# Performance work log

Measured on AMD Instinct MI355X. Metric: run time of the kernel, lower is better.

Reference implementation:

```python
import jax, jax.numpy as jnp
import numpy as np

N_FFT = 4096
HOP = 1024
WIN = 4096
DIAG_EPS = 1e-7
EPS = 1e-8

# asteroid-style periodic sqrt-hann analysis/synthesis window
_n = np.arange(WIN)
WINDOW = jnp.asarray(np.sqrt(0.5 - 0.5 * np.cos(2.0 * np.pi * _n / WIN)), dtype=jnp.float32)


def _frame_idx(n_samp):
    T = (n_samp - WIN) // HOP + 1
    return np.arange(T)[:, None] * HOP + np.arange(WIN)[None, :]


def stft(x):
    """x: (..., N) -> (real, imag) each (..., F, T) with F = N_FFT//2+1."""
    idx = _frame_idx(x.shape[-1])
    frames = x[..., idx] * WINDOW
    spec = jnp.fft.rfft(frames, axis=-1)     # (..., T, F) complex64
    spec = jnp.moveaxis(spec, -2, -1)        # (..., F, T)
    return spec.real, spec.imag


def istft(re, im, out_len):
    """(..., F, T) -> (..., out_len) via windowed overlap-add."""
    spec = jnp.moveaxis(re + 1j * im, -1, -2)            # (..., T, F)
    frames = jnp.fft.irfft(spec, n=WIN, axis=-1) * WINDOW
    T = frames.shape[-2]
    full = (T - 1) * HOP + WIN
    idx = _frame_idx(full).reshape(-1)
    flat = frames.reshape(frames.shape[:-2] + (-1,))
    out = jnp.zeros(frames.shape[:-2] + (full,), frames.dtype).at[..., idx].add(flat)
    wsq = jnp.zeros((full,), jnp.float32).at[idx].add(jnp.tile(WINDOW ** 2, T))
    out = out / jnp.maximum(wsq, 1e-8)
    return out[..., :out_len]


def psd_causal(re, im):
    """Causal, frame-normalized PSD. re/im: (B, C, F, T) -> complex (B, T, F, C, C)."""
    pr = jnp.einsum('saft,sbft->sabft', re, re) + jnp.einsum('saft,sbft->sabft', im, im)
    pi = jnp.einsum('saft,sbft->sbaft', re, im) - jnp.einsum('saft,sbft->sabft', re, im)
    cnt = jnp.arange(1, re.shape[-1] + 1, dtype=re.dtype)
    pr = jnp.cumsum(pr, -1) / cnt
    pi = jnp.cumsum(pi, -1) / cnt
    psd = pr + 1j * pi                       # (B, a, b, F, T)
    return jnp.transpose(psd, (0, 4, 3, 1, 2))  # (B, T, F, C, C)


def mvdr_vector(psd_s, psd_n):
    """Souden MVDR: ws = inv(Npsd) @ Spsd / (tr(.) + eps). (..., C, C) complex."""
    C = psd_n.shape[-1]
    tr_n = jnp.trace(psd_n, axis1=-2, axis2=-1).real
    epsilon = jax.lax.stop_gradient(tr_n * DIAG_EPS + EPS)
    psd_n = psd_n + epsilon[..., None, None] * jnp.eye(C, dtype=psd_n.dtype)
    num = jnp.linalg.inv(psd_n) @ psd_s
    return num / (jnp.trace(num, axis1=-2, axis2=-1)[..., None, None] + EPS)


def _forward(x, s):
    B, S, C, N = s.shape
    xs = jnp.broadcast_to(x[:, None], (B, S, C, N)).reshape(B * S, C, N)
    ss = s.reshape(B * S, C, N)
    Xr, Xi = stft(xs)
    Sr, Si = stft(ss)
    Nr, Ni = Xr - Sr, Xi - Si
    Sscm = psd_causal(Sr, Si)   # (BS, T, F, C, C)
    Nscm = psd_causal(Nr, Ni)
    ws = mvdr_vector(Sscm, Nscm)  # (BS, T, F, C, C)
    # conj(filter), rearranged to (BS, a, b, F, T)
    fr = jnp.transpose(ws.real, (0, 3, 4, 2, 1))
    fi = -jnp.transpose(ws.imag, (0, 3, 4, 2, 1))
    enh_r = jnp.einsum('sabft,saft->sbft', fr, Xr) - jnp.einsum('sabft,saft->sbft', fi, Xi)
    enh_i = jnp.einsum('sabft,saft->sbft', fr, Xi) + jnp.einsum('sabft,saft->sbft', fi, Xr)
    est = istft(enh_r, enh_i, N)            # (BS, C, N)
    return est.reshape(B, S, C, N)


def setup_inputs() -> dict:
    key = jax.random.key(0)
    kx, ks = jax.random.split(key)
    x = jax.random.normal(kx, (2, 4, 32768), dtype=jnp.float32)
    s = jax.random.normal(ks, (2, 2, 4, 32768), dtype=jnp.float32)
    return {"x": x, "s": s, "do_permute": 0}


def reference(x, s, do_permute):
    # do_permute=False path (PIT permutation is a data-dependent preprocessing step)
    return _forward(x, s)
```

## Files before the change

kernel.cpp:

```cpp
#include <hip/hip_runtime.h>

static constexpr int NFFT = 4096;
static constexpr int HOP  = 1024;
static constexpr int NF   = 2049;
static constexpr int NT   = 29;
static constexpr int NS   = 32768;
static constexpr int NB   = 2;
static constexpr int NSrc = 2;
static constexpr int NC   = 4;
static constexpr int NBS  = NB * NSrc;
static constexpr int FCHUNKS = (NF + 7) / 8;

#define PI_F     3.14159265358979323846f
#define TWO_PI_F 6.28318530717958647692f

#define IDX(a) ((a) + ((a) >> 4))
static constexpr int LDSN = 2048 + 128;

__device__ inline float2 cmul(float2 a, float2 b) {
    return make_float2(a.x * b.x - a.y * b.y, a.x * b.y + a.y * b.x);
}
__device__ inline float2 cmulc(float2 a, float2 b) {
    return make_float2(a.x * b.x + a.y * b.y, a.y * b.x - a.x * b.y);
}

template <int CTRL, int RMASK>
__device__ __forceinline__ float dpp0(float x) {
    return __int_as_float(__builtin_amdgcn_update_dpp(
        0, __float_as_int(x), CTRL, RMASK, 0xF, true));
}

template <int DIR>
__device__ inline void fft4v(float2 v[4]) {
    float2 t0 = make_float2(v[0].x + v[2].x, v[0].y + v[2].y);
    float2 t1 = make_float2(v[0].x - v[2].x, v[0].y - v[2].y);
    float2 t2 = make_float2(v[1].x + v[3].x, v[1].y + v[3].y);
    float2 t3 = make_float2(v[1].x - v[3].x, v[1].y - v[3].y);
    v[0] = make_float2(t0.x + t2.x, t0.y + t2.y);
    v[2] = make_float2(t0.x - t2.x, t0.y - t2.y);
    if (DIR < 0) {
        v[1] = make_float2(t1.x + t3.y, t1.y - t3.x);
        v[3] = make_float2(t1.x - t3.y, t1.y + t3.x);
    } else {
        v[1] = make_float2(t1.x - t3.y, t1.y + t3.x);
        v[3] = make_float2(t1.x + t3.y, t1.y - t3.x);
    }
}

template <int DIR>
__device__ inline void fft8v(float2 v[8]) {
    float2 e[4] = { v[0], v[2], v[4], v[6] };
    float2 o[4] = { v[1], v[3], v[5], v[7] };
    fft4v<DIR>(e);
    fft4v<DIR>(o);
    const float c = 0.70710678118654752f;
    float2 o0 = o[0], o1, o2, o3;
    if (DIR < 0) {
        o1 = make_float2(c * (o[1].x + o[1].y), c * (o[1].y - o[1].x));
        o2 = make_float2(o[2].y, -o[2].x);
        o3 = make_float2(c * (o[3].y - o[3].x), -c * (o[3].x + o[3].y));
    } else {
        o1 = make_float2(c * (o[1].x - o[1].y), c * (o[1].y + o[1].x));
        o2 = make_float2(-o[2].y, o[2].x);
        o3 = make_float2(-c * (o[3].x + o[3].y), c * (o[3].x - o[3].y));
    }
    v[0] = make_float2(e[0].x + o0.x, e[0].y + o0.y);
    v[4] = make_float2(e[0].x - o0.x, e[0].y - o0.y);
    v[1] = make_float2(e[1].x + o1.x, e[1].y + o1.y);
    v[5] = make_float2(e[1].x - o1.x, e[1].y - o1.y);
    v[2] = make_float2(e[2].x + o2.x, e[2].y + o2.y);
    v[6] = make_float2(e[2].x - o2.x, e[2].y - o2.y);
    v[3] = make_float2(e[3].x + o3.x, e[3].y + o3.y);
    v[7] = make_float2(e[3].x - o3.x, e[3].y - o3.y);
}

template <int DIR, int NSs>
__device__ inline void stage8(const float* __restrict__ reS, const float* __restrict__ imS,
                              float* __restrict__ reD, float* __restrict__ imD, int tid) {
    int j = tid;
    float2 v[8];
    #pragma unroll
    for (int r = 0; r < 8; ++r) {
        int a = IDX(j + (r << 8));
        v[r] = make_float2(reS[a], imS[a]);
    }
    if (NSs > 1) {
        float ang = (float)DIR * (TWO_PI_F / (8.0f * (float)NSs)) * (float)(j & (NSs - 1));
        float2 w1; __sincosf(ang, &w1.y, &w1.x);
        float2 w2 = cmul(w1, w1);
        float2 w3 = cmul(w2, w1);
        float2 w4 = cmul(w2, w2);
        float2 w5 = cmul(w3, w2);
        float2 w6 = cmul(w3, w3);
        float2 w7 = cmul(w4, w3);
        v[1] = cmul(v[1], w1);
        v[2] = cmul(v[2], w2);
        v[3] = cmul(v[3], w3);
        v[4] = cmul(v[4], w4);
        v[5] = cmul(v[5], w5);
        v[6] = cmul(v[6], w6);
        v[7] = cmul(v[7], w7);
    }
    fft8v<DIR>(v);
    int idxD = ((j & ~(NSs - 1)) << 3) + (j & (NSs - 1));
    #pragma unroll
    for (int r = 0; r < 8; ++r) {
        int a = IDX(idxD + r * NSs);
        reD[a] = v[r].x;
        imD[a] = v[r].y;
    }
}

template <int DIR>
__device__ inline void stage4_512(const float* __restrict__ reS, const float* __restrict__ imS,
                                  float* __restrict__ reD, float* __restrict__ imD, int tid) {
    #pragma unroll
    for (int h = 0; h < 2; ++h) {
        int j = tid + (h << 8);
        float2 v[4];
        #pragma unroll
        for (int r = 0; r < 4; ++r) {
            int a = IDX(j + (r << 9));
            v[r] = make_float2(reS[a], imS[a]);
        }
        float ang = (float)DIR * (TWO_PI_F / 2048.0f) * (float)j;
        float2 w1; __sincosf(ang, &w1.y, &w1.x);
        float2 w2 = cmul(w1, w1);
        float2 w3 = cmul(w2, w1);
        v[1] = cmul(v[1], w1);
        v[2] = cmul(v[2], w2);
        v[3] = cmul(v[3], w3);
        fft4v<DIR>(v);
        #pragma unroll
        for (int r = 0; r < 4; ++r) {
            int a = IDX(j + (r << 9));
            reD[a] = v[r].x;
            imD[a] = v[r].y;
        }
    }
}

template <int DIR>
__device__ inline void fft2048(float* reA, float* imA, float* reB, float* imB, int tid) {
    stage8<DIR, 1>(reA, imA, reB, imB, tid);  __syncthreads();
    stage8<DIR, 8>(reB, imB, reA, imA, tid);  __syncthreads();
    stage8<DIR, 64>(reA, imA, reB, imB, tid); __syncthreads();
    stage4_512<DIR>(reB, imB, reA, imA, tid); __syncthreads();
}

__global__ __launch_bounds__(256) void stft_kernel(
    const float* __restrict__ x, const float* __restrict__ s,
    float2* __restrict__ Xs, float2* __restrict__ Ss) {
    __shared__ float reA[LDSN], imA[LDSN], reB[LDSN], imB[LDSN];
    int tid = threadIdx.x;
    int fid = blockIdx.x;
    const float* src;
    float2* dst;
    if (fid < NB * NC * NT) {
        int b = fid / (NC * NT);
        int r = fid % (NC * NT);
        int c = r / NT;
        int t = r % NT;
        src = x + (size_t)((b * NC + c) * NS + t * HOP);
        dst = Xs + (size_t)((b * NC + c) * NT + t) * NF;
    } else {
        int g  = fid - NB * NC * NT;
        int bs = g / (NC * NT);
        int r  = g % (NC * NT);
        int c  = r / NT;
        int t  = r % NT;
        src = s + (size_t)((bs * NC + c) * NS + t * HOP);
        dst = Ss + (size_t)((bs * NC + c) * NT + t) * NF;
    }
    const float2* s2 = (const float2*)src;
    for (int n = tid; n < 2048; n += 256) {
        float2 v = s2[n];
        float we = __sinf((float)n * (PI_F / 2048.0f));
        float wo = __sinf((float)(2 * n + 1) * (PI_F / 4096.0f));
        int a = IDX(n);
        reA[a] = v.x * we;
        imA[a] = v.y * wo;
    }
    __syncthreads();
    fft2048<-1>(reA, imA, reB, imB, tid);
    for (int k = tid; k <= 1024; k += 256) {
        int a1 = IDX(k);
        int a2 = IDX((2048 - k) & 2047);
        float2 Za = make_float2(reA[a1], imA[a1]);
        float2 Zb = make_float2(reA[a2], imA[a2]);
        if (k == 0) {
            dst[0]    = make_float2(Za.x + Za.y, 0.f);
            dst[2048] = make_float2(Za.x - Za.y, 0.f);
        } else {
            float2 Ze = make_float2(0.5f * (Za.x + Zb.x),  0.5f * (Za.y - Zb.y));
            float2 Zo = make_float2(0.5f * (Za.y + Zb.y), -0.5f * (Za.x - Zb.x));
            float ang = -(PI_F / 2048.0f) * (float)k;
            float2 W; __sincosf(ang, &W.y, &W.x);
            float2 WZo = cmul(W, Zo);
            dst[k] = make_float2(Ze.x + WZo.x, Ze.y + WZo.y);
            if (k < 1024)
                dst[2048 - k] = make_float2(Ze.x - WZo.x, -(Ze.y - WZo.y));
        }
    }
}

__global__ __launch_bounds__(256) void mvdr2_kernel(
    const float2* __restrict__ Xs, const float2* __restrict__ Ss,
    float2* __restrict__ Es) {
    int tid   = threadIdx.x;
    int blk   = blockIdx.x;
    int bs    = blk / FCHUNKS;
    int f0    = (blk % FCHUNKS) * 8;
    int b     = bs >> 1;
    int lane  = tid & 63;
    int wave  = tid >> 6;
    int t     = lane & 31;
    int fpair = lane >> 5;
    int fi    = wave * 2 + fpair;
    int f     = f0 + fi;
    bool valid = (t < NT) && (f < NF);

    float2 Sv[4], Xv[4], Nv[4];
    #pragma unroll
    for (int c = 0; c < 4; ++c) {
        if (valid) {
            Sv[c] = Ss[(size_t)((bs * NC + c) * NT + t) * NF + f];
            Xv[c] = Xs[(size_t)((b  * NC + c) * NT + t) * NF + f];
        } else {
            Sv[c] = make_float2(0.f, 0.f);
            Xv[c] = make_float2(0.f, 0.f);
        }
        Nv[c] = make_float2(Xv[c].x - Sv[c].x, Xv[c].y - Sv[c].y);
    }

    float v[32];
    #pragma unroll
    for (int c = 0; c < 4; ++c) {
        v[c]      = Sv[c].x * Sv[c].x + Sv[c].y * Sv[c].y;
        v[16 + c] = Nv[c].x * Nv[c].x + Nv[c].y * Nv[c].y;
    }
    constexpr int PI6[6] = {0, 0, 0, 1, 1, 2};
    constexpr int PJ6[6] = {1, 2, 3, 2, 3, 3};
    #pragma unroll
    for (int p = 0; p < 6; ++p) {
        float2 d = cmulc(Sv[PI6[p]], Sv[PJ6[p]]);
        v[4 + 2 * p] = d.x; v[5 + 2 * p] = d.y;
        d = cmulc(Nv[PI6[p]], Nv[PJ6[p]]);
        v[20 + 2 * p] = d.x; v[21 + 2 * p] = d.y;
    }

    #pragma unroll
    for (int k = 0; k < 32; ++k) v[k] += dpp0<0x111, 0xF>(v[k]);
    #pragma unroll
    for (int k = 0; k < 32; ++k) v[k] += dpp0<0x112, 0xF>(v[k]);
    #pragma unroll
    for (int k = 0; k < 32; ++k) v[k] += dpp0<0x114, 0xF>(v[k]);
    #pragma unroll
    for (int k = 0; k < 32; ++k) v[k] += dpp0<0x118, 0xF>(v[k]);
    #pragma unroll
    for (int k = 0; k < 32; ++k) v[k] += dpp0<0x142, 0xA>(v[k]);

    float pd0 = v[0], pd1 = v[1], pd2 = v[2], pd3 = v[3];
    float2 po0 = make_float2(v[4],  v[5]);
    float2 po1 = make_float2(v[6],  v[7]);
    float2 po2 = make_float2(v[8],  v[9]);
    float2 po3 = make_float2(v[10], v[11]);
    float2 po4 = make_float2(v[12], v[13]);
    float2 po5 = make_float2(v[14], v[15]);
    float eps = (v[16] + v[17] + v[18] + v[19]) * 1e-7f + (float)(t + 1) * 1e-8f;
    float nd0 = v[16] + eps, nd1 = v[17] + eps, nd2 = v[18] + eps, nd3 = v[19] + eps;
    float2 no0 = make_float2(v[20], v[21]);
    float2 no1 = make_float2(v[22], v[23]);
    float2 no2 = make_float2(v[24], v[25]);
    float2 no3 = make_float2(v[26], v[27]);
    float2 no4 = make_float2(v[28], v[29]);
    float2 no5 = make_float2(v[30], v[31]);

    float D0 = nd0;
    float r0 = __builtin_amdgcn_rcpf(D0);
    float2 L10 = make_float2(no0.x * r0, -no0.y * r0);
    float2 L20 = make_float2(no1.x * r0, -no1.y * r0);
    float2 L30 = make_float2(no2.x * r0, -no2.y * r0);
    float D1 = nd1 - (L10.x * L10.x + L10.y * L10.y) * D0;
    float r1 = __builtin_amdgcn_rcpf(D1);
    float2 c10 = make_float2(D0 * L10.x, -D0 * L10.y);
    float2 tA = cmul(L20, c10);
    float2 L21 = make_float2((no3.x - tA.x) * r1, (-no3.y - tA.y) * r1);
    float2 tB = cmul(L30, c10);
    float2 L31 = make_float2((no4.x - tB.x) * r1, (-no4.y - tB.y) * r1);
    float D2 = nd2 - (L20.x * L20.x + L20.y * L20.y) * D0
                   - (L21.x * L21.x + L21.y * L21.y) * D1;
    float r2 = __builtin_amdgcn_rcpf(D2);
    float2 c20 = make_float2(D0 * L20.x, -D0 * L20.y);
    float2 c21 = make_float2(D1 * L21.x, -D1 * L21.y);
    float2 tC = cmul(L30, c20);
    float2 tD = cmul(L31, c21);
    float2 L32 = make_float2((no5.x - tC.x - tD.x) * r2, (-no5.y - tC.y - tD.y) * r2);
    float D3 = nd3 - (L30.x * L30.x + L30.y * L30.y) * D0
                   - (L31.x * L31.x + L31.y * L31.y) * D1
                   - (L32.x * L32.x + L32.y * L32.y) * D2;
    float r3 = __builtin_amdgcn_rcpf(D3);

    float2 u0 = Xv[0];
    float2 m0 = cmul(L10, u0);
    float2 u1 = make_float2(Xv[1].x - m0.x, Xv[1].y - m0.y);
    float2 m1 = cmul(L20, u0), m2 = cmul(L21, u1);
    float2 u2 = make_float2(Xv[2].x - m1.x - m2.x, Xv[2].y - m1.y - m2.y);
    float2 m3 = cmul(L30, u0), m4 = cmul(L31, u1), m5 = cmul(L32, u2);
    float2 u3 = make_float2(Xv[3].x - m3.x - m4.x - m5.x,
                            Xv[3].y - m3.y - m4.y - m5.y);
    float2 w0 = make_float2(u0.x * r0, u0.y * r0);
    float2 w1 = make_float2(u1.x * r1, u1.y * r1);
    float2 w2 = make_float2(u2.x * r2, u2.y * r2);
    float2 w3 = make_float2(u3.x * r3, u3.y * r3);
    float2 z3 = w3;
    float2 n0_ = cmulc(z3, L32);
    float2 z2 = make_float2(w2.x - n0_.x, w2.y - n0_.y);
    float2 n1_ = cmulc(z2, L21), n2_ = cmulc(z3, L31);
    float2 z1 = make_float2(w1.x - n1_.x - n2_.x, w1.y - n1_.y - n2_.y);
    float2 n3_ = cmulc(z1, L10), n4_ = cmulc(z2, L20), n5_ = cmulc(z3, L30);
    float2 z0 = make_float2(w0.x - n3_.x - n4_.x - n5_.x,
                            w0.y - n3_.y - n4_.y - n5_.y);

    float2 K10 = make_float2(-L10.x, -L10.y);
    float2 kk  = cmul(L21, L10);
    float2 K20 = make_float2(kk.x - L20.x, kk.y - L20.y);
    float2 K21 = make_float2(-L21.x, -L21.y);
    kk = cmul(L32, L21);
    float2 K31 = make_float2(kk.x - L31.x, kk.y - L31.y);
    float2 K32 = make_float2(-L32.x, -L32.y);
    float2 ka = cmul(K31, L10), kb = cmul(L32, L20);
    float2 K30 = make_float2(-L30.x - ka.x + kb.x, -L30.y - ka.y + kb.y);

    float q0 = pd0;
    float2 qm = cmul(K10, po0);
    float q1 = pd1 + (K10.x * K10.x + K10.y * K10.y) * pd0 + 2.0f * qm.x;
    qm = cmul(K20, po0);
    float s_a = qm.x * K21.x + qm.y * K21.y;
    qm = cmul(K20, po1);
    float s_b = qm.x;
    qm = cmul(K21, po3);
    float s_c = qm.x;
    float q2 = pd2 + (K20.x * K20.x + K20.y * K20.y) * pd0
                   + (K21.x * K21.x + K21.y * K21.y) * pd1
                   + 2.0f * (s_a + s_b + s_c);
    qm = cmul(K30, po0);
    float s1 = qm.x * K31.x + qm.y * K31.y;
    qm = cmul(K30, po1);
    float s2 = qm.x * K32.x + qm.y * K32.y;
    qm = cmul(K30, po2);
    float s3 = qm.x;
    qm = cmul(K31, po3);
    float s4 = qm.x * K32.x + qm.y * K32.y;
    qm = cmul(K31, po4);
    float s5 = qm.x;
    qm = cmul(K32, po5);
    float s6 = qm.x;
    float q3 = pd3 + (K30.x * K30.x + K30.y * K30.y) * pd0
                   + (K31.x * K31.x + K31.y * K31.y) * pd1
                   + (K32.x * K32.x + K32.y * K32.y) * pd2
                   + 2.0f * (s1 + s2 + s3 + s4 + s5 + s6);
    float tr = q0 * r0 + q1 * r1 + q2 * r2 + q3 * r3;
    float g  = __builtin_amdgcn_rcpf(tr + 1e-8f);

    float2 a0 = cmul(po0, z1), a1 = cmul(po1, z2), a2 = cmul(po2, z3);
    float2 e0 = make_float2(pd0 * z0.x + a0.x + a1.x + a2.x,
                            pd0 * z0.y + a0.y + a1.y + a2.y);
    a0 = cmulc(z0, po0); a1 = cmul(po3, z2); a2 = cmul(po4, z3);
    float2 e1 = make_float2(a0.x + pd1 * z1.x + a1.x + a2.x,
                            a0.y + pd1 * z1.y + a1.y + a2.y);
    a0 = cmulc(z0, po1); a1 = cmulc(z1, po3); a2 = cmul(po5, z3);
    float2 e2 = make_float2(a0.x + a1.x + pd2 * z2.x + a2.x,
                            a0.y + a1.y + pd2 * z2.y + a2.y);
    a0 = cmulc(z0, po2); a1 = cmulc(z1, po4); a2 = cmulc(z2, po5);
    float2 e3 = make_float2(a0.x + a1.x + a2.x + pd3 * z3.x,
                            a0.y + a1.y + a2.y + pd3 * z3.y);
    if (valid) {
        Es[(size_t)((bs * NC + 0) * NT + t) * NF + f] = make_float2(e0.x * g, e0.y * g);
        Es[(size_t)((bs * NC + 1) * NT + t) * NF + f] = make_float2(e1.x * g, e1.y * g);
        Es[(size_t)((bs * NC + 2) * NT + t) * NF + f] = make_float2(e2.x * g, e2.y * g);
        Es[(size_t)((bs * NC + 3) * NT + t) * NF + f] = make_float2(e3.x * g, e3.y * g);
    }
}

__global__ __launch_bounds__(256) void istft_kernel(
    const float2* __restrict__ Es, float* __restrict__ Fr) {
    __shared__ float reA[LDSN], imA[LDSN], reB[LDSN], imB[LDSN];
    int tid = threadIdx.x;
    int fid = blockIdx.x;
    int bs = fid / (NC * NT);
    int r  = fid % (NC * NT);
    int c  = r / NT;
    int t  = r % NT;
    const float2* src = Es + (size_t)((bs * NC + c) * NT + t) * NF;
    for (int k = tid; k <= 1024; k += 256) {
        float2 A = src[k];
        float2 B = src[2048 - k];
        float2 Ze = make_float2(0.5f * (A.x + B.x), 0.5f * (A.y - B.y));
        float2 D  = make_float2(0.5f * (A.x - B.x), 0.5f * (A.y + B.y));
        float ang = (PI_F / 2048.0f) * (float)k;
        float2 W; __sincosf(ang, &W.y, &W.x);
        float2 Zo = cmul(W, D);
        int a1 = IDX(k);
        reA[a1] = Ze.x - Zo.y;
        imA[a1] = Ze.y + Zo.x;
        if (k > 0 && k < 1024) {
            int a2 = IDX(2048 - k);
            reA[a2] = Ze.x + Zo.y;
            imA[a2] = -Ze.y + Zo.x;
        }
    }
    __syncthreads();
    fft2048<1>(reA, imA, reB, imB, tid);
    float2* d2 = (float2*)(Fr + (size_t)((bs * NC + c) * NT + t) * NFFT);
    for (int n = tid; n < 2048; n += 256) {
        int a = IDX(n);
        float we = __sinf((float)n * (PI_F / 2048.0f)) * (1.0f / 2048.0f);
        float wo = __sinf((float)(2 * n + 1) * (PI_F / 4096.0f)) * (1.0f / 2048.0f);
        d2[n] = make_float2(reA[a] * we, imA[a] * wo);
    }
}

__global__ __launch_bounds__(256) void ola_kernel(
    const float* __restrict__ Fr, float* __restrict__ out) {
    int idx = blockIdx.x * 256 + threadIdx.x;
    const int total = NBS * NC * NS;
    if (idx >= total) return;
    int p  = idx & (NS - 1);
    int ch = idx >> 15;
    int t1 = p >> 10;
    if (t1 > NT - 1) t1 = NT - 1;
    int t0 = (p >= NFFT) ? ((p - (NFFT - 1) + (HOP - 1)) >> 10) : 0;
    float acc = 0.f;
    for (int t = t0; t <= t1; ++t)
        acc += Fr[((size_t)(ch * NT + t) << 12) + (p - (t << 10))];
    float wacc;
    if (t1 - t0 == 3) {
        wacc = 2.0f;
    } else {
        wacc = 0.f;
        for (int t = t0; t <= t1; ++t) {
            float w = __sinf((float)(p - (t << 10)) * (PI_F / 4096.0f));
            wacc += w * w;
        }
    }
    out[idx] = acc / fmaxf(wacc, 1e-8f);
}

extern "C" void kernel_launch(void* const* d_in, const int* in_sizes, int n_in,
                              void* d_out, int out_size, void* d_ws, size_t ws_size,
                              hipStream_t stream) {
    const float* x = (const float*)d_in[0];
    const float* s = (const float*)d_in[1];
    float* out = (float*)d_out;

    const size_t XS_N = (size_t)NB  * NC * NT * NF;
    const size_t SS_N = (size_t)NBS * NC * NT * NF;
    float2* Xs = (float2*)d_ws;
    float2* Ss = Xs + XS_N;
    float2* Es = Ss + SS_N;
    float*  Fr = (float*)(Es + SS_N);

    stft_kernel<<<NB * NC * NT + NBS * NC * NT, 256, 0, stream>>>(x, s, Xs, Ss);

    mvdr2_kernel<<<NBS * FCHUNKS, 256, 0, stream>>>(Xs, Ss, Es);

    istft_kernel<<<NBS * NC * NT, 256, 0, stream>>>(Es, Fr);

    int ola_total = NBS * NC * NS;
    ola_kernel<<<(ola_total + 255) / 256, 256, 0, stream>>>(Fr, out);
}
```

Measured before the change: 37.33 us.

## Pad spectra to even bin stride and process two bins per thread in MVDR

Spectra buffers now use a padded row stride of 2050 bins, so each MVDR thread can load and store two adjacent frequency bins with 16-byte vector accesses. The MVDR kernel is restructured to handle 16 bins per block, with the solve factored into a helper that runs twice per thread. This halves the block count and widens memory transactions, at the cost of doubled register pressure (64 reduction values) and a launch bound that may limit occupancy. It risks spilling and has fewer blocks to hide latency.

Result: slower. 38.11 us (+2.1%).

```diff
diff --git a/kernel.cpp b/kernel.cpp
--- a/kernel.cpp
+++ b/kernel.cpp
@@ -3,13 +3,14 @@
 static constexpr int NFFT = 4096;
 static constexpr int HOP  = 1024;
 static constexpr int NF   = 2049;
+static constexpr int NF2  = 2050;
 static constexpr int NT   = 29;
 static constexpr int NS   = 32768;
 static constexpr int NB   = 2;
 static constexpr int NSrc = 2;
 static constexpr int NC   = 4;
 static constexpr int NBS  = NB * NSrc;
-static constexpr int FCHUNKS = (NF + 7) / 8;
+static constexpr int FCH16 = 129;
 
 #define PI_F     3.14159265358979323846f
 #define TWO_PI_F 6.28318530717958647692f
@@ -162,7 +163,7 @@
         int c = r / NT;
         int t = r % NT;
         src = x + (size_t)((b * NC + c) * NS + t * HOP);
-        dst = Xs + (size_t)((b * NC + c) * NT + t) * NF;
+        dst = Xs + (size_t)((b * NC + c) * NT + t) * NF2;
     } else {
         int g  = fid - NB * NC * NT;
         int bs = g / (NC * NT);
@@ -170,7 +171,7 @@
         int c  = r / NT;
         int t  = r % NT;
         src = s + (size_t)((bs * NC + c) * NS + t * HOP);
-        dst = Ss + (size_t)((bs * NC + c) * NT + t) * NF;
+        dst = Ss + (size_t)((bs * NC + c) * NT + t) * NF2;
     }
     const float2* s2 = (const float2*)src;
     for (int n = tid; n < 2048; n += 256) {
@@ -204,62 +205,9 @@
     }
 }
 
-__global__ __launch_bounds__(256) void mvdr2_kernel(
-    const float2* __restrict__ Xs, const float2* __restrict__ Ss,
-    float2* __restrict__ Es) {
-    int tid   = threadIdx.x;
-    int blk   = blockIdx.x;
-    int bs    = blk / FCHUNKS;
-    int f0    = (blk % FCHUNKS) * 8;
-    int b     = bs >> 1;
-    int lane  = tid & 63;
-    int wave  = tid >> 6;
-    int t     = lane & 31;
-    int fpair = lane >> 5;
-    int fi    = wave * 2 + fpair;
-    int f     = f0 + fi;
-    bool valid = (t < NT) && (f < NF);
-
-    float2 Sv[4], Xv[4], Nv[4];
-    #pragma unroll
-    for (int c = 0; c < 4; ++c) {
-        if (valid) {
-            Sv[c] = Ss[(size_t)((bs * NC + c) * NT + t) * NF + f];
-            Xv[c] = Xs[(size_t)((b  * NC + c) * NT + t) * NF + f];
-        } else {
-            Sv[c] = make_float2(0.f, 0.f);
-            Xv[c] = make_float2(0.f, 0.f);
-        }
-        Nv[c] = make_float2(Xv[c].x - Sv[c].x, Xv[c].y - Sv[c].y);
-    }
-
-    float v[32];
-    #pragma unroll
-    for (int c = 0; c < 4; ++c) {
-        v[c]      = Sv[c].x * Sv[c].x + Sv[c].y * Sv[c].y;
-        v[16 + c] = Nv[c].x * Nv[c].x + Nv[c].y * Nv[c].y;
-    }
-    constexpr int PI6[6] = {0, 0, 0, 1, 1, 2};
-    constexpr int PJ6[6] = {1, 2, 3, 2, 3, 3};
-    #pragma unroll
-    for (int p = 0; p < 6; ++p) {
-        float2 d = cmulc(Sv[PI6[p]], Sv[PJ6[p]]);
-        v[4 + 2 * p] = d.x; v[5 + 2 * p] = d.y;
-        d = cmulc(Nv[PI6[p]], Nv[PJ6[p]]);
-        v[20 + 2 * p] = d.x; v[21 + 2 * p] = d.y;
-    }
-
-    #pragma unroll
-    for (int k = 0; k < 32; ++k) v[k] += dpp0<0x111, 0xF>(v[k]);
-    #pragma unroll
-    for (int k = 0; k < 32; ++k) v[k] += dpp0<0x112, 0xF>(v[k]);
-    #pragma unroll
-    for (int k = 0; k < 32; ++k) v[k] += dpp0<0x114, 0xF>(v[k]);
-    #pragma unroll
-    for (int k = 0; k < 32; ++k) v[k] += dpp0<0x118, 0xF>(v[k]);
-    #pragma unroll
-    for (int k = 0; k < 32; ++k) v[k] += dpp0<0x142, 0xA>(v[k]);
-
+__device__ __forceinline__ void mvdr_solve(const float* __restrict__ v,
+                                           const float2* __restrict__ Xv,
+                                           int t, float2* __restrict__ e) {
     float pd0 = v[0], pd1 = v[1], pd2 = v[2], pd3 = v[3];
     float2 po0 = make_float2(v[4],  v[5]);
     float2 po1 = make_float2(v[6],  v[7]);
@@ -364,22 +312,106 @@
     float g  = __builtin_amdgcn_rcpf(tr + 1e-8f);
 
     float2 a0 = cmul(po0, z1), a1 = cmul(po1, z2), a2 = cmul(po2, z3);
-    float2 e0 = make_float2(pd0 * z0.x + a0.x + a1.x + a2.x,
-                            pd0 * z0.y + a0.y + a1.y + a2.y);
+    e[0] = make_float2((pd0 * z0.x + a0.x + a1.x + a2.x) * g,
+                       (pd0 * z0.y + a0.y + a1.y + a2.y) * g);
     a0 = cmulc(z0, po0); a1 = cmul(po3, z2); a2 = cmul(po4, z3);
-    float2 e1 = make_float2(a0.x + pd1 * z1.x + a1.x + a2.x,
-                            a0.y + pd1 * z1.y + a1.y + a2.y);
+    e[1] = make_float2((a0.x + pd1 * z1.x + a1.x + a2.x) * g,
+                       (a0.y + pd1 * z1.y + a1.y + a2.y) * g);
     a0 = cmulc(z0, po1); a1 = cmulc(z1, po3); a2 = cmul(po5, z3);
-    float2 e2 = make_float2(a0.x + a1.x + pd2 * z2.x + a2.x,
-                            a0.y + a1.y + pd2 * z2.y + a2.y);
+    e[2] = make_float2((a0.x + a1.x + pd2 * z2.x + a2.x) * g,
+                       (a0.y + a1.y + pd2 * z2.y + a2.y) * g);
     a0 = cmulc(z0, po2); a1 = cmulc(z1, po4); a2 = cmulc(z2, po5);
-    float2 e3 = make_float2(a0.x + a1.x + a2.x + pd3 * z3.x,
-                            a0.y + a1.y + a2.y + pd3 * z3.y);
-    if (valid) {
-        Es[(size_t)((bs * NC + 0) * NT + t) * NF + f] = make_float2(e0.x * g, e0.y * g);
-        Es[(size_t)((bs * NC + 1) * NT + t) * NF + f] = make_float2(e1.x * g, e1.y * g);
-        Es[(size_t)((bs * NC + 2) * NT + t) * NF + f] = make_float2(e2.x * g, e2.y * g);
-        Es[(size_t)((bs * NC + 3) * NT + t) * NF + f] = make_float2(e3.x * g, e3.y * g);
+    e[3] = make_float2((a0.x + a1.x + a2.x + pd3 * z3.x) * g,
+                       (a0.y + a1.y + a2.y + pd3 * z3.y) * g);
+}
+
+__global__ __launch_bounds__(256, 1) void mvdr2_kernel(
+    const float2* __restrict__ Xs, const float2* __restrict__ Ss,
+    float2* __restrict__ Es) {
+    int tid   = threadIdx.x;
+    int blk   = blockIdx.x;
+    int bs    = blk / FCH16;
+    int f0    = (blk % FCH16) * 16;
+    int b     = bs >> 1;
+    int lane  = tid & 63;
+    int wave  = tid >> 6;
+    int t     = lane & 31;
+    int fpair = lane >> 5;
+    int fA    = f0 + (wave * 2 + fpair) * 2;
+    bool loadok = (t < NT) && (fA <= 2048);
+
+    float2 SvA[4], SvB[4], XvA[4], XvB[4];
+    #pragma unroll
+    for (int c = 0; c < 4; ++c) {
+        if (loadok) {
+            float4 qs = *(const float4*)&Ss[(size_t)((bs * NC + c) * NT + t) * NF2 + fA];
+            float4 qx = *(const float4*)&Xs[(size_t)((b  * NC + c) * NT + t) * NF2 + fA];
+            SvA[c] = make_float2(qs.x, qs.y);
+            SvB[c] = make_float2(qs.z, qs.w);
+            XvA[c] = make_float2(qx.x, qx.y);
+            XvB[c] = make_float2(qx.z, qx.w);
+        } else {
+            SvA[c] = make_float2(0.f, 0.f);
+            SvB[c] = make_float2(0.f, 0.f);
+            XvA[c] = make_float2(0.f, 0.f);
+            XvB[c] = make_float2(0.f, 0.f);
+        }
+    }
+    float2 NvA[4], NvB[4];
+    #pragma unroll
+    for (int c = 0; c < 4; ++c) {
+        NvA[c] = make_float2(XvA[c].x - SvA[c].x, XvA[c].y - SvA[c].y);
+        NvB[c] = make_float2(XvB[c].x - SvB[c].x, XvB[c].y - SvB[c].y);
+    }
+
+    float v[64];
+    #pragma unroll
+    for (int c = 0; c < 4; ++c) {
+        v[c]      = SvA[c].x * SvA[c].x + SvA[c].y * SvA[c].y;
+        v[16 + c] = NvA[c].x * NvA[c].x + NvA[c].y * NvA[c].y;
+        v[32 + c] = SvB[c].x * SvB[c].x + SvB[c].y * SvB[c].y;
+        v[48 + c] = NvB[c].x * NvB[c].x + NvB[c].y * NvB[c].y;
+    }
+    constexpr int PI6[6] = {0, 0, 0, 1, 1, 2};
+    constexpr int PJ6[6] = {1, 2, 3, 2, 3, 3};
+    #pragma unroll
+    for (int p = 0; p < 6; ++p) {
+        float2 d = cmulc(SvA[PI6[p]], SvA[PJ6[p]]);
+        v[4 + 2 * p] = d.x;  v[5 + 2 * p] = d.y;
+        d = cmulc(NvA[PI6[p]], NvA[PJ6[p]]);
+        v[20 + 2 * p] = d.x; v[21 + 2 * p] = d.y;
+        d = cmulc(SvB[PI6[p]], SvB[PJ6[p]]);
+        v[36 + 2 * p] = d.x; v[37 + 2 * p] = d.y;
+        d = cmulc(NvB[PI6[p]], NvB[PJ6[p]]);
+        v[52 + 2 * p] = d.x; v[53 + 2 * p] = d.y;
+    }
+
+    #pragma unroll
+    for (int k = 0; k < 64; ++k) v[k] += dpp0<0x111, 0xF>(v[k]);
+    #pragma unroll
+    for (int k = 0; k < 64; ++k) v[k] += dpp0<0x112, 0xF>(v[k]);
+    #pragma unroll
+    for (int k = 0; k < 64; ++k) v[k] += dpp0<0x114, 0xF>(v[k]);
+    #pragma unroll
+    for (int k = 0; k < 64; ++k) v[k] += dpp0<0x118, 0xF>(v[k]);
+    #pragma unroll
+    for (int k = 0; k < 64; ++k) v[k] += dpp0<0x142, 0xA>(v[k]);
+
+    float2 eA[4], eB[4];
+    mvdr_solve(v,      XvA, t, eA);
+    mvdr_solve(v + 32, XvB, t, eB);
+
+    if (t < NT) {
+        if (fA + 1 <= 2048) {
+            #pragma unroll
+            for (int bo = 0; bo < 4; ++bo)
+                *(float4*)&Es[(size_t)((bs * NC + bo) * NT + t) * NF2 + fA] =
+                    make_float4(eA[bo].x, eA[bo].y, eB[bo].x, eB[bo].y);
+        } else if (fA <= 2048) {
+            #pragma unroll
+            for (int bo = 0; bo < 4; ++bo)
+                Es[(size_t)((bs * NC + bo) * NT + t) * NF2 + fA] = eA[bo];
+        }
     }
 }
 
@@ -392,7 +424,7 @@
     int r  = fid % (NC * NT);
     int c  = r / NT;
     int t  = r % NT;
-    const float2* src = Es + (size_t)((bs * NC + c) * NT + t) * NF;
+    const float2* src = Es + (size_t)((bs * NC + c) * NT + t) * NF2;
     for (int k = tid; k <= 1024; k += 256) {
         float2 A = src[k];
         float2 B = src[2048 - k];
@@ -454,16 +486,17 @@
     const float* s = (const float*)d_in[1];
     float* out = (float*)d_out;
 
-    const size_t XS_N = (size_t)NB  * NC * NT * NF;
-    const size_t SS_N = (size_t)NBS * NC * NT * NF;
+    const size_t XS_N = (size_t)NB  * NC * NT * NF2;
+    const size_t SS_N = (size_t)NBS * NC * NT * NF2;
+    const size_t ES_N = (size_t)NBS * NC * NT * NF2;
     float2* Xs = (float2*)d_ws;
     float2* Ss = Xs + XS_N;
     float2* Es = Ss + SS_N;
-    float*  Fr = (float*)(Es + SS_N);
+    float*  Fr = (float*)(Es + ES_N);
 
     stft_kernel<<<NB * NC * NT + NBS * NC * NT, 256, 0, stream>>>(x, s, Xs, Ss);
 
-    mvdr2_kernel<<<NBS * FCHUNKS, 256, 0, stream>>>(Xs, Ss, Es);
+    mvdr2_kernel<<<NBS * FCH16, 256, 0, stream>>>(Xs, Ss, Es);
 
     istft_kernel<<<NBS * NC * NT, 256, 0, stream>>>(Es, Fr);
 
```
